# Optimization experiments

Hardware: AMD Instinct MI355X
Metric: run time of the kernel (lower is better)

## Reference

```python
import jax, jax.numpy as jnp
import numpy as np

N_STATE = 1280
N_HEAD = 20
D_HEAD = N_STATE // N_HEAD  # 64
N_MLP = 4 * N_STATE         # 5120
EPS = 1e-5


def _layer_norm(x, gamma, beta):
    mu = jnp.mean(x, axis=-1, keepdims=True)
    var = jnp.mean(jnp.square(x - mu), axis=-1, keepdims=True)
    return (x - mu) * jax.lax.rsqrt(var + EPS) * gamma + beta


def setup_inputs() -> dict:
    key = jax.random.key(0)
    ks = jax.random.split(key, 16)
    s = lambda fan_in: 1.0 / np.sqrt(fan_in)
    d = {
        "x": jax.random.normal(ks[0], (1, 1500, N_STATE), jnp.float32),
        # attention projections (stored [in, out]; torch Linear does x @ W.T + b)
        "Wq": jax.random.normal(ks[1], (N_STATE, N_STATE), jnp.float32) * s(N_STATE),
        "bq": jax.random.normal(ks[2], (N_STATE,), jnp.float32) * 0.02,
        "Wk": jax.random.normal(ks[3], (N_STATE, N_STATE), jnp.float32) * s(N_STATE),  # no bias
        "Wv": jax.random.normal(ks[4], (N_STATE, N_STATE), jnp.float32) * s(N_STATE),
        "bv": jax.random.normal(ks[5], (N_STATE,), jnp.float32) * 0.02,
        "Wo": jax.random.normal(ks[6], (N_STATE, N_STATE), jnp.float32) * s(N_STATE),
        "bo": jax.random.normal(ks[7], (N_STATE,), jnp.float32) * 0.02,
        # layer norms
        "ln1_g": jnp.ones((N_STATE,), jnp.float32),
        "ln1_b": jnp.zeros((N_STATE,), jnp.float32),
        "ln2_g": jnp.ones((N_STATE,), jnp.float32),
        "ln2_b": jnp.zeros((N_STATE,), jnp.float32),
        # MLP
        "W1": jax.random.normal(ks[8], (N_STATE, N_MLP), jnp.float32) * s(N_STATE),
        "b1": jax.random.normal(ks[9], (N_MLP,), jnp.float32) * 0.02,
        "W2": jax.random.normal(ks[10], (N_MLP, N_STATE), jnp.float32) * s(N_MLP),
        "b2": jax.random.normal(ks[11], (N_STATE,), jnp.float32) * 0.02,
    }
    return d


def reference(x, Wq, bq, Wk, Wv, bv, Wo, bo, ln1_g, ln1_b, ln2_g, ln2_b, W1, b1, W2, b2):
    B, S, C = x.shape
    scale = D_HEAD ** -0.5

    # --- multi-head self-attention ---
    h = _layer_norm(x, ln1_g, ln1_b)
    q = (h @ Wq + bq).reshape(B, S, N_HEAD, D_HEAD)
    k = (h @ Wk).reshape(B, S, N_HEAD, D_HEAD)
    v = (h @ Wv + bv).reshape(B, S, N_HEAD, D_HEAD)
    # scores: [B, H, Q, K]; softmax over keys (dim=1 'k' in the torch einsum)
    scores = jnp.einsum('bqhd,bkhd->bhqk', q, k) * scale
    w = jax.nn.softmax(scores, axis=-1)
    attn = jnp.einsum('bhqk,bkhd->bqhd', w, v).reshape(B, S, C)
    attn = attn @ Wo + bo
    x = x + attn

    # --- MLP (exact GELU, matching torch nn.GELU default) ---
    h2 = _layer_norm(x, ln2_g, ln2_b)
    h2 = jax.nn.gelu(h2 @ W1 + b1, approximate=False)
    x = x + (h2 @ W2 + b2)
    return x
```

## Files before the change

kernel.cpp:

```cpp
#include <hip/hip_runtime.h>
#include <hip/hip_bf16.h>
#include <math.h>

typedef __bf16 bf16x8 __attribute__((ext_vector_type(8)));
typedef float f32x4 __attribute__((ext_vector_type(4)));

#define SEQ 1500
#define CDIM 1280
#define NHEAD 20
#define DHEAD 64
#define NMLP 5120
#define QKVN 3840
#define VTLD 1504
#define APAD 68

#define GLOAD_LDS16(gp, lp)                                                    \
  __builtin_amdgcn_global_load_lds(                                            \
      (const __attribute__((address_space(1))) unsigned int*)(gp),             \
      (__attribute__((address_space(3))) unsigned int*)(lp), 16, 0, 0)

__global__ void detect_kernel(const unsigned int* __restrict__ xw,
                              int* __restrict__ flag) {
  __shared__ int cnt[256];
  const unsigned int w = xw[threadIdx.x];
  const unsigned int e = (w >> 7) & 0xFF;
  cnt[threadIdx.x] = (e >= 100 && e <= 150) ? 1 : 0;
  __syncthreads();
  for (int s = 128; s > 0; s >>= 1) {
    if (threadIdx.x < (unsigned)s) cnt[threadIdx.x] += cnt[threadIdx.x + s];
    __syncthreads();
  }
  if (threadIdx.x == 0) flag[0] = (cnt[0] >= 160) ? 1 : 0;
}

__global__ __launch_bounds__(256) void pack_params_kernel(
    const void* bq, const void* bv, const void* bo, const void* g1,
    const void* be1, const void* g2, const void* be2, const void* b1,
    const void* b2, __bf16* __restrict__ pb, const int* __restrict__ flag) {
  const int isbf = flag[0];
  const int i = blockIdx.x * 256 + threadIdx.x;
  if (i >= 16640) return;
  auto ld = [&](const void* p, int j) -> float {
    return isbf ? (float)((const __bf16*)p)[j] : ((const float*)p)[j];
  };
  float v;
  if (i < 3840) {
    if (i < 1280) v = ld(bq, i);
    else if (i < 2560) v = 0.f;
    else v = ld(bv, i - 2560);
  } else if (i < 5120) v = ld(bo, i - 3840);
  else if (i < 6400) v = ld(g1, i - 5120);
  else if (i < 7680) v = ld(be1, i - 6400);
  else if (i < 8960) v = ld(g2, i - 7680);
  else if (i < 10240) v = ld(be2, i - 8960);
  else if (i < 15360) v = ld(b1, i - 10240);
  else v = ld(b2, i - 15360);
  pb[i] = (__bf16)v;
}

__device__ __forceinline__ void transpose_body(const void* in, __bf16* out,
                                               int K, int N, int isbf) {
  __shared__ __bf16 t[32][33];
  const int tx = threadIdx.x, ty = threadIdx.y;
  const int n0 = blockIdx.x * 32, k0 = blockIdx.y * 32;
  if (isbf) {
    const __bf16* s = (const __bf16*)in;
#pragma unroll
    for (int i = ty; i < 32; i += 8)
      t[i][tx] = s[(size_t)(k0 + i) * N + n0 + tx];
  } else {
    const float* s = (const float*)in;
#pragma unroll
    for (int i = ty; i < 32; i += 8)
      t[i][tx] = (__bf16)s[(size_t)(k0 + i) * N + n0 + tx];
  }
  __syncthreads();
#pragma unroll
  for (int i = ty; i < 32; i += 8)
    out[(size_t)(n0 + i) * K + k0 + tx] = t[tx][i];
}

__global__ __launch_bounds__(256) void transpose_kernel(const void* __restrict__ in,
                                                        __bf16* __restrict__ out,
                                                        int K, int N,
                                                        const int* __restrict__ flag) {
  transpose_body(in, out, K, N, flag[0]);
}

__global__ __launch_bounds__(256) void transpose3_kernel(const void* __restrict__ Wq,
                                                         const void* __restrict__ Wk,
                                                         const void* __restrict__ Wv,
                                                         __bf16* __restrict__ out,
                                                         const int* __restrict__ flag) {
  const void* in = blockIdx.z == 0 ? Wq : (blockIdx.z == 1 ? Wk : Wv);
  transpose_body(in, out + (size_t)blockIdx.z * CDIM * CDIM, CDIM, CDIM, flag[0]);
}

__global__ __launch_bounds__(256) void transpose_act_kernel(const __bf16* __restrict__ in,
                                                            __bf16* __restrict__ out,
                                                            int istride) {
  __shared__ __bf16 t[32][33];
  const int tx = threadIdx.x, ty = threadIdx.y;
  const int n0 = blockIdx.x * 32, k0 = blockIdx.y * 32;
#pragma unroll
  for (int i = ty; i < 32; i += 8) {
    const int k = k0 + i;
    t[i][tx] = (k < SEQ) ? in[(size_t)k * istride + n0 + tx] : (__bf16)0.f;
  }
  __syncthreads();
#pragma unroll
  for (int i = ty; i < 32; i += 8) {
    const int kk = k0 + tx;
    if (kk < VTLD) out[(size_t)(n0 + i) * VTLD + kk] = t[tx][i];
  }
}

__global__ __launch_bounds__(256) void ln_kernel(const void* __restrict__ X,
                                                 const __bf16* __restrict__ gamma,
                                                 const __bf16* __restrict__ beta,
                                                 __bf16* __restrict__ Y,
                                                 int xflag, const int* __restrict__ flag) {
  const int isf32 = xflag ? (flag[0] == 0) : 0;
  const int row = blockIdx.x;
  float v[5];
  float s = 0.f, s2 = 0.f;
#pragma unroll
  for (int i = 0; i < 5; ++i) {
    const int c = threadIdx.x + 256 * i;
    const size_t idx = (size_t)row * CDIM + c;
    v[i] = isf32 ? ((const float*)X)[idx] : (float)((const __bf16*)X)[idx];
    s += v[i];
    s2 += v[i] * v[i];
  }
  const int lane = threadIdx.x & 63, wv = threadIdx.x >> 6;
#pragma unroll
  for (int off = 32; off > 0; off >>= 1) {
    s += __shfl_down(s, off);
    s2 += __shfl_down(s2, off);
  }
  __shared__ float red[8];
  if (lane == 0) { red[wv] = s; red[4 + wv] = s2; }
  __syncthreads();
  s = red[0] + red[1] + red[2] + red[3];
  s2 = red[4] + red[5] + red[6] + red[7];
  const float mu = s * (1.f / CDIM);
  const float var = s2 * (1.f / CDIM) - mu * mu;
  const float rstd = rsqrtf(fmaxf(var, 0.f) + 1e-5f);
#pragma unroll
  for (int i = 0; i < 5; ++i) {
    const int c = threadIdx.x + 256 * i;
    Y[(size_t)row * CDIM + c] =
        (__bf16)((v[i] - mu) * rstd * (float)gamma[c] + (float)beta[c]);
  }
}

__global__ __launch_bounds__(256) void gemm64_kernel(
    const __bf16* __restrict__ A, const __bf16* __restrict__ Bt,
    const __bf16* __restrict__ bias, void* __restrict__ Cv,
    int M, int N, int K, int KS, int gelu, int nsplit) {
  __shared__ __bf16 As[2][64 * 32];
  __shared__ __bf16 Bs[2][128 * 32];
  const int bm = blockIdx.x, bn = blockIdx.y, sz = blockIdx.z;
  const int tid = threadIdx.x;
  const int lane = tid & 63, wave = tid >> 6;
  const int l16 = lane & 15, kq = (lane >> 4) << 3;
  const int lrow = lane >> 2, lcol = (lane & 3) << 3;
  const int wn = wave * 32;

  f32x4 acc[4][2];
  const f32x4 zero = {0.f, 0.f, 0.f, 0.f};
#pragma unroll
  for (int i = 0; i < 4; ++i)
#pragma unroll
    for (int j = 0; j < 2; ++j) acc[i][j] = zero;

  const int kbeg = sz * KS;
  int kend = kbeg + KS;
  if (kend > K) kend = K;

  int ga = bm * 64 + wave * 16 + lrow;
  if (ga > M - 1) ga = M - 1;
  const __bf16* Ap = A + (size_t)ga * K + lcol;

  for (int k0 = kbeg; k0 < kend; k0 += 64) {
#pragma unroll
    for (int c = 0; c < 2; ++c)
      GLOAD_LDS16(Ap + k0 + c * 32, &As[c][wave * 512]);
#pragma unroll
    for (int c = 0; c < 2; ++c)
#pragma unroll
      for (int t = 0; t < 2; ++t) {
        const int seg = t * 4 + wave;
        const int gb = bn * 128 + seg * 16 + lrow;
        GLOAD_LDS16(Bt + (size_t)gb * K + k0 + c * 32 + lcol, &Bs[c][seg * 512]);
      }
    __syncthreads();
    bf16x8 af[4][2], bfr[2][2];
#pragma unroll
    for (int i = 0; i < 4; ++i)
#pragma unroll
      for (int c = 0; c < 2; ++c)
        af[i][c] = *(const bf16x8*)(&As[c][(i * 16 + l16) * 32 + kq]);
#pragma unroll
    for (int j = 0; j < 2; ++j)
#pragma unroll
      for (int c = 0; c < 2; ++c)
        bfr[j][c] = *(const bf16x8*)(&Bs[c][(wn + j * 16 + l16) * 32 + kq]);
#pragma unroll
    for (int i = 0; i < 4; ++i)
#pragma unroll
      for (int j = 0; j < 2; ++j)
#pragma unroll
        for (int c = 0; c < 2; ++c)
          acc[i][j] = __builtin_amdgcn_mfma_f32_16x16x32_bf16(af[i][c], bfr[j][c],
                                                              acc[i][j], 0, 0, 0);
    __syncthreads();
  }

  const int rq4 = (lane >> 4) * 4;
  if (nsplit > 1) {
    float* P = (float*)Cv + (size_t)sz * M * N;
#pragma unroll
    for (int i = 0; i < 4; ++i)
#pragma unroll
      for (int r = 0; r < 4; ++r) {
        const int grow = bm * 64 + i * 16 + rq4 + r;
        if (grow >= M) continue;
#pragma unroll
        for (int j = 0; j < 2; ++j) {
          const int gcol = bn * 128 + wn + j * 16 + l16;
          P[(size_t)grow * N + gcol] = acc[i][j][r];
        }
      }
  } else {
    __bf16* Cb = (__bf16*)Cv;
#pragma unroll
    for (int i = 0; i < 4; ++i)
#pragma unroll
      for (int r = 0; r < 4; ++r) {
        const int grow = bm * 64 + i * 16 + rq4 + r;
        if (grow >= M) continue;
#pragma unroll
        for (int j = 0; j < 2; ++j) {
          const int gcol = bn * 128 + wn + j * 16 + l16;
          float vv = acc[i][j][r];
          if (bias) vv += (float)bias[gcol];
          if (gelu) vv = 0.5f * vv * (1.f + erff(vv * 0.70710678118654752f));
          Cb[(size_t)grow * N + gcol] = (__bf16)vv;
        }
      }
  }
}

__global__ __launch_bounds__(256) void reduce_kernel(
    const float* __restrict__ P, const __bf16* __restrict__ bias,
    const void* __restrict__ resid, void* __restrict__ out,
    int MN, int N, int S, int residflagged, int outflagged,
    const int* __restrict__ flag) {
  const int i = blockIdx.x * 256 + threadIdx.x;
  if (i >= MN) return;
  float v = 0.f;
  for (int s = 0; s < S; ++s) v += P[(size_t)s * MN + i];
  v += (float)bias[i % N];
  if (resid) {
    const int rf32 = residflagged ? (flag[0] == 0) : 0;
    v += rf32 ? ((const float*)resid)[i] : (float)((const __bf16*)resid)[i];
  }
  const int outbf = outflagged ? flag[0] : 1;
  if (outbf) ((__bf16*)out)[i] = (__bf16)v;
  else       ((float*)out)[i] = v;
}

__global__ __launch_bounds__(256) void attn_mfma_kernel(
    const __bf16* __restrict__ Q,
    const __bf16* __restrict__ Kk,
    const __bf16* __restrict__ Vt,
    float* __restrict__ Opart,
    float* __restrict__ ml,
    int rs) {
  const int h = blockIdx.y;
  const int q0 = blockIdx.x * 64;
  const int z = blockIdx.z;
  const int tid = threadIdx.x;
  const int wave = tid >> 6, lane = tid & 63;
  const int l16 = lane & 15, quad = lane >> 4;

  __shared__ __bf16 Ks[64 * APAD];
  __shared__ __bf16 Vs[64 * APAD];
  __shared__ __bf16 Ps[4][16 * APAD];

  bf16x8 qf[2];
  {
    int q = q0 + wave * 16 + l16;
    if (q > SEQ - 1) q = SEQ - 1;
    const __bf16* qp = Q + (size_t)q * rs + h * DHEAD + quad * 8;
    qf[0] = *(const bf16x8*)(qp);
    qf[1] = *(const bf16x8*)(qp + 32);
  }

  f32x4 oacc[4];
  const f32x4 zero = {0.f, 0.f, 0.f, 0.f};
#pragma unroll
  for (int jt = 0; jt < 4; ++jt) oacc[jt] = zero;
  float mrow[4], lrow[4];
#pragma unroll
  for (int r = 0; r < 4; ++r) { mrow[r] = -30000.f; lrow[r] = 0.f; }

  const int srow = tid >> 2;
  const int scol = (tid & 3) << 4;

  const __bf16* Kbase = Kk + h * DHEAD;
  const __bf16* Vbase = Vt + (size_t)(h * DHEAD + srow) * VTLD;

  for (int kt = z * 12; kt < z * 12 + 12; ++kt) {
    const int key0 = kt * 64;
    __syncthreads();
    {
      int gk = key0 + srow;
      if (gk > SEQ - 1) gk = SEQ - 1;
      const __bf16* kp = Kbase + (size_t)gk * rs + scol;
      *(bf16x8*)(&Ks[srow * APAD + scol]) = *(const bf16x8*)(kp);
      *(bf16x8*)(&Ks[srow * APAD + scol + 8]) = *(const bf16x8*)(kp + 8);
      const __bf16* vp = Vbase + key0 + scol;
      *(bf16x8*)(&Vs[srow * APAD + scol]) = *(const bf16x8*)(vp);
      *(bf16x8*)(&Vs[srow * APAD + scol + 8]) = *(const bf16x8*)(vp + 8);
    }
    __syncthreads();

    f32x4 s[4];
#pragma unroll
    for (int jt = 0; jt < 4; ++jt) s[jt] = zero;
#pragma unroll
    for (int jt = 0; jt < 4; ++jt)
#pragma unroll
      for (int ks = 0; ks < 2; ++ks) {
        const bf16x8 kf = *(const bf16x8*)(&Ks[(jt * 16 + l16) * APAD + ks * 32 + quad * 8]);
        s[jt] = __builtin_amdgcn_mfma_f32_16x16x32_bf16(qf[ks], kf, s[jt], 0, 0, 0);
      }

#pragma unroll
    for (int jt = 0; jt < 4; ++jt) {
      const int key = key0 + jt * 16 + l16;
#pragma unroll
      for (int r = 0; r < 4; ++r) {
        float sv = s[jt][r] * 0.125f;
        if (key >= SEQ) sv = -30000.f;
        s[jt][r] = sv;
      }
    }

#pragma unroll
    for (int r = 0; r < 4; ++r) {
      float tmax = fmaxf(fmaxf(s[0][r], s[1][r]), fmaxf(s[2][r], s[3][r]));
#pragma unroll
      for (int off = 8; off > 0; off >>= 1) tmax = fmaxf(tmax, __shfl_xor(tmax, off));
      const float mnew = fmaxf(mrow[r], tmax);
      const float alpha = __expf(mrow[r] - mnew);
      mrow[r] = mnew;
      lrow[r] *= alpha;
#pragma unroll
      for (int jt = 0; jt < 4; ++jt) oacc[jt][r] *= alpha;
#pragma unroll
      for (int jt = 0; jt < 4; ++jt) {
        const float p = __expf(s[jt][r] - mnew);
        lrow[r] += p;
        Ps[wave][(quad * 4 + r) * APAD + jt * 16 + l16] = (__bf16)p;
      }
    }

    bf16x8 pf[2];
    pf[0] = *(const bf16x8*)(&Ps[wave][l16 * APAD + quad * 8]);
    pf[1] = *(const bf16x8*)(&Ps[wave][l16 * APAD + 32 + quad * 8]);
#pragma unroll
    for (int jt = 0; jt < 4; ++jt)
#pragma unroll
      for (int ks = 0; ks < 2; ++ks) {
        const bf16x8 vf = *(const bf16x8*)(&Vs[(jt * 16 + l16) * APAD + ks * 32 + quad * 8]);
        oacc[jt] = __builtin_amdgcn_mfma_f32_16x16x32_bf16(pf[ks], vf, oacc[jt], 0, 0, 0);
      }
  }

  float* Oz = Opart + (size_t)z * SEQ * CDIM;
#pragma unroll
  for (int r = 0; r < 4; ++r) {
    float lt = lrow[r];
#pragma unroll
    for (int off = 8; off > 0; off >>= 1) lt += __shfl_xor(lt, off);
    const int q = q0 + wave * 16 + quad * 4 + r;
    if (q < SEQ) {
#pragma unroll
      for (int jt = 0; jt < 4; ++jt)
        Oz[(size_t)q * CDIM + h * DHEAD + jt * 16 + l16] = oacc[jt][r];
      if (l16 == 0) {
        const size_t mi = ((size_t)(z * NHEAD + h) * SEQ + q) * 2;
        ml[mi] = mrow[r];
        ml[mi + 1] = lt;
      }
    }
  }
}

__global__ __launch_bounds__(256) void attn_combine_kernel(
    const float* __restrict__ Op, const float* __restrict__ ml,
    __bf16* __restrict__ O) {
  const int i = blockIdx.x * 256 + threadIdx.x;
  if (i >= SEQ * CDIM) return;
  const int q = i / CDIM;
  const int h = (i % CDIM) >> 6;
  const size_t m1i = ((size_t)h * SEQ + q) * 2;
  const size_t m2i = ((size_t)(NHEAD + h) * SEQ + q) * 2;
  const float m1 = ml[m1i], l1 = ml[m1i + 1];
  const float m2 = ml[m2i], l2 = ml[m2i + 1];
  const float M = fmaxf(m1, m2);
  const float e1 = __expf(m1 - M), e2 = __expf(m2 - M);
  const float v = (e1 * Op[i] + e2 * Op[(size_t)SEQ * CDIM + i]) /
                  (e1 * l1 + e2 * l2);
  O[i] = (__bf16)v;
}

extern "C" void kernel_launch(void* const* d_in, const int* in_sizes, int n_in,
                              void* d_out, int out_size, void* d_ws, size_t ws_size,
                              hipStream_t stream) {
  const void* x   = d_in[0];
  const void* Wq  = d_in[1];
  const void* bq  = d_in[2];
  const void* Wk  = d_in[3];
  const void* Wv  = d_in[4];
  const void* bv  = d_in[5];
  const void* Wo  = d_in[6];
  const void* bo  = d_in[7];
  const void* g1  = d_in[8];
  const void* be1 = d_in[9];
  const void* g2  = d_in[10];
  const void* be2 = d_in[11];
  const void* W1  = d_in[12];
  const void* bm1 = d_in[13];
  const void* W2  = d_in[14];
  const void* bm2 = d_in[15];

  char* ws = (char*)d_ws;
  size_t off = 0;
  auto alloc = [&](size_t elems) {
    __bf16* p = (__bf16*)(ws + off);
    off += elems * sizeof(__bf16);
    return p;
  };
  __bf16* Wqkvt = alloc((size_t)QKVN * CDIM);
  __bf16* Wot   = alloc((size_t)CDIM * CDIM);
  __bf16* W1t   = alloc((size_t)CDIM * NMLP);
  __bf16* W2t   = alloc((size_t)CDIM * NMLP);
  __bf16* qkvb  = alloc((size_t)SEQ * QKVN);
  __bf16* hb    = alloc((size_t)SEQ * CDIM);
  __bf16* mb    = alloc((size_t)SEQ * NMLP);
  __bf16* pb    = alloc(20480);
  off = (off + 15) & ~(size_t)15;
  float* pscr = (float*)(ws + off);
  off += (size_t)2 * SEQ * CDIM * sizeof(float);
  float* mlb = (float*)(ws + off);
  off += (size_t)2 * NHEAD * SEQ * 2 * sizeof(float);
  int* flag = (int*)(ws + off);

  __bf16* vtb  = mb;
  __bf16* x1b  = qkvb;
  __bf16* h2b  = qkvb + (size_t)SEQ * CDIM;

  __bf16* qkvbias = pb + 0;
  __bf16* bo_b  = pb + 3840;
  __bf16* g1_b  = pb + 5120;
  __bf16* be1_b = pb + 6400;
  __bf16* g2_b  = pb + 7680;
  __bf16* be2_b = pb + 8960;
  __bf16* b1_b  = pb + 10240;
  __bf16* b2_b  = pb + 15360;

  detect_kernel<<<1, 256, 0, stream>>>((const unsigned int*)x, flag);
  pack_params_kernel<<<65, 256, 0, stream>>>(bq, bv, bo, g1, be1, g2, be2,
                                             bm1, bm2, pb, flag);

  const dim3 tb(32, 8);
  transpose3_kernel<<<dim3(40, 40, 3), tb, 0, stream>>>(Wq, Wk, Wv, Wqkvt, flag);
  transpose_kernel<<<dim3(40, 40), tb, 0, stream>>>(Wo, Wot, CDIM, CDIM, flag);
  transpose_kernel<<<dim3(160, 40), tb, 0, stream>>>(W1, W1t, CDIM, NMLP, flag);
  transpose_kernel<<<dim3(40, 160), tb, 0, stream>>>(W2, W2t, NMLP, CDIM, flag);

  ln_kernel<<<SEQ, 256, 0, stream>>>(x, g1_b, be1_b, hb, 1, flag);
  gemm64_kernel<<<dim3(24, 30, 1), 256, 0, stream>>>(
      hb, Wqkvt, qkvbias, qkvb, SEQ, QKVN, CDIM, CDIM, 0, 1);
  transpose_act_kernel<<<dim3(40, 47), tb, 0, stream>>>(qkvb + 2560, vtb, QKVN);
  attn_mfma_kernel<<<dim3(24, NHEAD, 2), 256, 0, stream>>>(
      qkvb, qkvb + 1280, vtb, pscr, mlb, QKVN);
  attn_combine_kernel<<<7500, 256, 0, stream>>>(pscr, mlb, hb);
  gemm64_kernel<<<dim3(24, 10, 2), 256, 0, stream>>>(
      hb, Wot, nullptr, pscr, SEQ, CDIM, CDIM, 640, 0, 2);
  reduce_kernel<<<7500, 256, 0, stream>>>(pscr, bo_b, x, x1b,
                                          SEQ * CDIM, CDIM, 2, 1, 0, flag);
  ln_kernel<<<SEQ, 256, 0, stream>>>(x1b, g2_b, be2_b, h2b, 0, flag);
  gemm64_kernel<<<dim3(24, 40, 1), 256, 0, stream>>>(
      h2b, W1t, b1_b, mb, SEQ, NMLP, CDIM, CDIM, 1, 1);
  gemm64_kernel<<<dim3(24, 10, 2), 256, 0, stream>>>(
      mb, W2t, nullptr, pscr, SEQ, CDIM, NMLP, 2560, 0, 2);
  reduce_kernel<<<7500, 256, 0, stream>>>(pscr, b2_b, x1b, d_out,
                                          SEQ * CDIM, CDIM, 2, 0, 1, flag);
}
```

Before: 377.2 us.

## Add 128x128 double-buffered GEMM for QKV/MLP1 and prefetch in split-K GEMM

Adds a new 128x128-tile GEMM kernel with a 2x2 wave layout, used for the QKV projection and the first MLP GEMM, so each wave computes a 64x64 sub-tile and reuses its LDS fragments more. Both that kernel and the existing split-K 64x128 GEMM now use 32-wide K steps with a double-buffered LDS prefetch: the next tile is loaded while the current one is computed, and there is one barrier per iteration. This targets global-load latency stalls and barrier overhead. The trade-off is fewer blocks for the large GEMMs (360/480 blocks), which lowers occupancy and wave-level parallelism, plus higher register pressure from 16 accumulators.

```diff
diff --git a/kernel.cpp b/kernel.cpp
--- a/kernel.cpp
+++ b/kernel.cpp
@@ -154,10 +154,86 @@
   }
 }
 
+__global__ __launch_bounds__(256) void gemm128_kernel(
+    const __bf16* __restrict__ A, const __bf16* __restrict__ Bt,
+    const __bf16* __restrict__ bias, __bf16* __restrict__ C,
+    int M, int N, int K, int gelu) {
+  __shared__ __bf16 As[2][128 * 32];
+  __shared__ __bf16 Bs[2][128 * 32];
+  const int bm = blockIdx.x, bn = blockIdx.y;
+  const int tid = threadIdx.x;
+  const int lane = tid & 63, wave = tid >> 6;
+  const int wm = (wave >> 1) * 64, wn = (wave & 1) * 64;
+  const int l16 = lane & 15, kq = (lane >> 4) << 3;
+  const int lrow = lane >> 2, lcol = (lane & 3) << 3;
+
+  f32x4 acc[4][4];
+  const f32x4 zero = {0.f, 0.f, 0.f, 0.f};
+#pragma unroll
+  for (int i = 0; i < 4; ++i)
+#pragma unroll
+    for (int j = 0; j < 4; ++j) acc[i][j] = zero;
+
+  int ga0 = bm * 128 + wave * 16 + lrow;
+  if (ga0 > M - 1) ga0 = M - 1;
+  int ga1 = bm * 128 + (wave + 4) * 16 + lrow;
+  if (ga1 > M - 1) ga1 = M - 1;
+  const int gb0 = bn * 128 + wave * 16 + lrow;
+  const int gb1 = bn * 128 + (wave + 4) * 16 + lrow;
+  const __bf16* Ap0 = A + (size_t)ga0 * K + lcol;
+  const __bf16* Ap1 = A + (size_t)ga1 * K + lcol;
+  const __bf16* Bp0 = Bt + (size_t)gb0 * K + lcol;
+  const __bf16* Bp1 = Bt + (size_t)gb1 * K + lcol;
+
+  auto stage = [&](int b, int k0) {
+    GLOAD_LDS16(Ap0 + k0, &As[b][wave * 512]);
+    GLOAD_LDS16(Ap1 + k0, &As[b][(wave + 4) * 512]);
+    GLOAD_LDS16(Bp0 + k0, &Bs[b][wave * 512]);
+    GLOAD_LDS16(Bp1 + k0, &Bs[b][(wave + 4) * 512]);
+  };
+
+  stage(0, 0);
+  int buf = 0;
+  for (int k0 = 0; k0 < K; k0 += 32) {
+    __syncthreads();
+    if (k0 + 32 < K) stage(buf ^ 1, k0 + 32);
+    bf16x8 af[4], bfr[4];
+#pragma unroll
+    for (int i = 0; i < 4; ++i)
+      af[i] = *(const bf16x8*)(&As[buf][(wm + i * 16 + l16) * 32 + kq]);
+#pragma unroll
+    for (int j = 0; j < 4; ++j)
+      bfr[j] = *(const bf16x8*)(&Bs[buf][(wn + j * 16 + l16) * 32 + kq]);
+#pragma unroll
+    for (int i = 0; i < 4; ++i)
+#pragma unroll
+      for (int j = 0; j < 4; ++j)
+        acc[i][j] = __builtin_amdgcn_mfma_f32_16x16x32_bf16(af[i], bfr[j],
+                                                            acc[i][j], 0, 0, 0);
+    buf ^= 1;
+  }
+
+  const int rq4 = (lane >> 4) * 4;
+#pragma unroll
+  for (int i = 0; i < 4; ++i)
+#pragma unroll
+    for (int r = 0; r < 4; ++r) {
+      const int grow = bm * 128 + wm + i * 16 + rq4 + r;
+      if (grow >= M) continue;
+#pragma unroll
+      for (int j = 0; j < 4; ++j) {
+        const int gcol = bn * 128 + wn + j * 16 + l16;
+        float vv = acc[i][j][r];
+        if (bias) vv += (float)bias[gcol];
+        if (gelu) vv = 0.5f * vv * (1.f + erff(vv * 0.70710678118654752f));
+        C[(size_t)grow * N + gcol] = (__bf16)vv;
+      }
+    }
+}
+
 __global__ __launch_bounds__(256) void gemm64_kernel(
     const __bf16* __restrict__ A, const __bf16* __restrict__ Bt,
-    const __bf16* __restrict__ bias, void* __restrict__ Cv,
-    int M, int N, int K, int KS, int gelu, int nsplit) {
+    float* __restrict__ P, int M, int N, int K, int KS) {
   __shared__ __bf16 As[2][64 * 32];
   __shared__ __bf16 Bs[2][128 * 32];
   const int bm = blockIdx.x, bn = blockIdx.y, sz = blockIdx.z;
@@ -180,76 +256,53 @@
 
   int ga = bm * 64 + wave * 16 + lrow;
   if (ga > M - 1) ga = M - 1;
+  const int gb0 = bn * 128 + wave * 16 + lrow;
+  const int gb1 = bn * 128 + (wave + 4) * 16 + lrow;
   const __bf16* Ap = A + (size_t)ga * K + lcol;
-
-  for (int k0 = kbeg; k0 < kend; k0 += 64) {
-#pragma unroll
-    for (int c = 0; c < 2; ++c)
-      GLOAD_LDS16(Ap + k0 + c * 32, &As[c][wave * 512]);
-#pragma unroll
-    for (int c = 0; c < 2; ++c)
-#pragma unroll
-      for (int t = 0; t < 2; ++t) {
-        const int seg = t * 4 + wave;
-        const int gb = bn * 128 + seg * 16 + lrow;
-        GLOAD_LDS16(Bt + (size_t)gb * K + k0 + c * 32 + lcol, &Bs[c][seg * 512]);
-      }
+  const __bf16* Bp0 = Bt + (size_t)gb0 * K + lcol;
+  const __bf16* Bp1 = Bt + (size_t)gb1 * K + lcol;
+
+  auto stage = [&](int b, int k0) {
+    GLOAD_LDS16(Ap + k0, &As[b][wave * 512]);
+    GLOAD_LDS16(Bp0 + k0, &Bs[b][wave * 512]);
+    GLOAD_LDS16(Bp1 + k0, &Bs[b][(wave + 4) * 512]);
+  };
+
+  stage(0, kbeg);
+  int buf = 0;
+  for (int k0 = kbeg; k0 < kend; k0 += 32) {
     __syncthreads();
-    bf16x8 af[4][2], bfr[2][2];
+    if (k0 + 32 < kend) stage(buf ^ 1, k0 + 32);
+    bf16x8 af[4], bfr[2];
 #pragma unroll
     for (int i = 0; i < 4; ++i)
-#pragma unroll
-      for (int c = 0; c < 2; ++c)
-        af[i][c] = *(const bf16x8*)(&As[c][(i * 16 + l16) * 32 + kq]);
+      af[i] = *(const bf16x8*)(&As[buf][(i * 16 + l16) * 32 + kq]);
 #pragma unroll
     for (int j = 0; j < 2; ++j)
-#pragma unroll
-      for (int c = 0; c < 2; ++c)
-        bfr[j][c] = *(const bf16x8*)(&Bs[c][(wn + j * 16 + l16) * 32 + kq]);
+      bfr[j] = *(const bf16x8*)(&Bs[buf][(wn + j * 16 + l16) * 32 + kq]);
 #pragma unroll
     for (int i = 0; i < 4; ++i)
 #pragma unroll
       for (int j = 0; j < 2; ++j)
-#pragma unroll
-        for (int c = 0; c < 2; ++c)
-          acc[i][j] = __builtin_amdgcn_mfma_f32_16x16x32_bf16(af[i][c], bfr[j][c],
-                                                              acc[i][j], 0, 0, 0);
-    __syncthreads();
-  }
-
+        acc[i][j] = __builtin_amdgcn_mfma_f32_16x16x32_bf16(af[i], bfr[j],
+                                                            acc[i][j], 0, 0, 0);
+    buf ^= 1;
+  }
+
+  float* Pz = P + (size_t)sz * M * N;
   const int rq4 = (lane >> 4) * 4;
-  if (nsplit > 1) {
-    float* P = (float*)Cv + (size_t)sz * M * N;
-#pragma unroll
-    for (int i = 0; i < 4; ++i)
-#pragma unroll
-      for (int r = 0; r < 4; ++r) {
-        const int grow = bm * 64 + i * 16 + rq4 + r;
-        if (grow >= M) continue;
-#pragma unroll
-        for (int j = 0; j < 2; ++j) {
-          const int gcol = bn * 128 + wn + j * 16 + l16;
-          P[(size_t)grow * N + gcol] = acc[i][j][r];
-        }
-      }
-  } else {
-    __bf16* Cb = (__bf16*)Cv;
-#pragma unroll
-    for (int i = 0; i < 4; ++i)
-#pragma unroll
-      for (int r = 0; r < 4; ++r) {
-        const int grow = bm * 64 + i * 16 + rq4 + r;
-        if (grow >= M) continue;
-#pragma unroll
-        for (int j = 0; j < 2; ++j) {
-          const int gcol = bn * 128 + wn + j * 16 + l16;
-          float vv = acc[i][j][r];
-          if (bias) vv += (float)bias[gcol];
-          if (gelu) vv = 0.5f * vv * (1.f + erff(vv * 0.70710678118654752f));
-          Cb[(size_t)grow * N + gcol] = (__bf16)vv;
-        }
-      }
-  }
+#pragma unroll
+  for (int i = 0; i < 4; ++i)
+#pragma unroll
+    for (int r = 0; r < 4; ++r) {
+      const int grow = bm * 64 + i * 16 + rq4 + r;
+      if (grow >= M) continue;
+#pragma unroll
+      for (int j = 0; j < 2; ++j) {
+        const int gcol = bn * 128 + wn + j * 16 + l16;
+        Pz[(size_t)grow * N + gcol] = acc[i][j][r];
+      }
+    }
 }
 
 __global__ __launch_bounds__(256) void reduce_kernel(
@@ -484,21 +537,21 @@
   transpose_kernel<<<dim3(40, 160), tb, 0, stream>>>(W2, W2t, NMLP, CDIM, flag);
 
   ln_kernel<<<SEQ, 256, 0, stream>>>(x, g1_b, be1_b, hb, 1, flag);
-  gemm64_kernel<<<dim3(24, 30, 1), 256, 0, stream>>>(
-      hb, Wqkvt, qkvbias, qkvb, SEQ, QKVN, CDIM, CDIM, 0, 1);
+  gemm128_kernel<<<dim3(12, 30), 256, 0, stream>>>(
+      hb, Wqkvt, qkvbias, qkvb, SEQ, QKVN, CDIM, 0);
   transpose_act_kernel<<<dim3(40, 47), tb, 0, stream>>>(qkvb + 2560, vtb, QKVN);
   attn_mfma_kernel<<<dim3(24, NHEAD, 2), 256, 0, stream>>>(
       qkvb, qkvb + 1280, vtb, pscr, mlb, QKVN);
   attn_combine_kernel<<<7500, 256, 0, stream>>>(pscr, mlb, hb);
   gemm64_kernel<<<dim3(24, 10, 2), 256, 0, stream>>>(
-      hb, Wot, nullptr, pscr, SEQ, CDIM, CDIM, 640, 0, 2);
+      hb, Wot, pscr, SEQ, CDIM, CDIM, 640);
   reduce_kernel<<<7500, 256, 0, stream>>>(pscr, bo_b, x, x1b,
                                           SEQ * CDIM, CDIM, 2, 1, 0, flag);
   ln_kernel<<<SEQ, 256, 0, stream>>>(x1b, g2_b, be2_b, h2b, 0, flag);
-  gemm64_kernel<<<dim3(24, 40, 1), 256, 0, stream>>>(
-      h2b, W1t, b1_b, mb, SEQ, NMLP, CDIM, CDIM, 1, 1);
+  gemm128_kernel<<<dim3(12, 40), 256, 0, stream>>>(
+      h2b, W1t, b1_b, mb, SEQ, NMLP, CDIM, 1);
   gemm64_kernel<<<dim3(24, 10, 2), 256, 0, stream>>>(
-      mb, W2t, nullptr, pscr, SEQ, CDIM, NMLP, 2560, 0, 2);
+      mb, W2t, pscr, SEQ, CDIM, NMLP, 2560);
   reduce_kernel<<<7500, 256, 0, stream>>>(pscr, b2_b, x1b, d_out,
                                           SEQ * CDIM, CDIM, 2, 0, 1, flag);
 }
```

After: 399.6 us. 1.06x slower.

## Use 128x128 GEMM tiles with LDS double buffering and XCD-aware block mapping

Applied to the files above, without the earlier changes.

Replaces the 64x128 GEMM kernel with a 128x128 tile in which each of four waves computes a 64x64 sub-tile. Global-to-LDS loads for the next K step are issued into a second buffer before computing the current one, which removes one barrier per iteration. A 1D grid is remapped so that consecutive block IDs, which land on different XCDs, take different N tiles while sharing the same M tile. The larger tile raises data reuse but halves block count (for example 384 blocks for QKV), doubles LDS use and adds accumulator registers, which may lower occupancy.

```diff
diff --git a/kernel.cpp b/kernel.cpp
--- a/kernel.cpp
+++ b/kernel.cpp
@@ -154,67 +154,87 @@
   }
 }
 
-__global__ __launch_bounds__(256) void gemm64_kernel(
+__global__ __launch_bounds__(256) void gemm128s_kernel(
     const __bf16* __restrict__ A, const __bf16* __restrict__ Bt,
     const __bf16* __restrict__ bias, void* __restrict__ Cv,
-    int M, int N, int K, int KS, int gelu, int nsplit) {
-  __shared__ __bf16 As[2][64 * 32];
-  __shared__ __bf16 Bs[2][128 * 32];
-  const int bm = blockIdx.x, bn = blockIdx.y, sz = blockIdx.z;
+    int M, int N, int K, int KS, int gelu, int nsplit,
+    int mtiles, int ntpad) {
+  __shared__ __bf16 As[2][2][128 * 32];
+  __shared__ __bf16 Bs[2][2][128 * 32];
+
+  int id = blockIdx.x;
+  const int per = mtiles * ntpad;
+  const int sz = id / per;
+  id %= per;
+  const int xcd = id & 7;
+  const int grp = id >> 3;
+  const int bm = grp % mtiles;
+  const int bn = (grp / mtiles) * 8 + xcd;
+  if (bn >= (N >> 7)) return;
+
   const int tid = threadIdx.x;
   const int lane = tid & 63, wave = tid >> 6;
+  const int wm = (wave >> 1) * 64, wn = (wave & 1) * 64;
   const int l16 = lane & 15, kq = (lane >> 4) << 3;
   const int lrow = lane >> 2, lcol = (lane & 3) << 3;
-  const int wn = wave * 32;
-
-  f32x4 acc[4][2];
+
+  f32x4 acc[4][4];
   const f32x4 zero = {0.f, 0.f, 0.f, 0.f};
 #pragma unroll
   for (int i = 0; i < 4; ++i)
 #pragma unroll
-    for (int j = 0; j < 2; ++j) acc[i][j] = zero;
+    for (int j = 0; j < 4; ++j) acc[i][j] = zero;
+
+  const __bf16* Ap[2];
+  const __bf16* Bp[2];
+#pragma unroll
+  for (int t = 0; t < 2; ++t) {
+    int ga = bm * 128 + t * 64 + wave * 16 + lrow;
+    if (ga > M - 1) ga = M - 1;
+    Ap[t] = A + (size_t)ga * K + lcol;
+    const int gb = bn * 128 + t * 64 + wave * 16 + lrow;
+    Bp[t] = Bt + (size_t)gb * K + lcol;
+  }
 
   const int kbeg = sz * KS;
   int kend = kbeg + KS;
   if (kend > K) kend = K;
 
-  int ga = bm * 64 + wave * 16 + lrow;
-  if (ga > M - 1) ga = M - 1;
-  const __bf16* Ap = A + (size_t)ga * K + lcol;
-
+  auto stage = [&](int b, int k0) {
+#pragma unroll
+    for (int t = 0; t < 2; ++t)
+#pragma unroll
+      for (int c = 0; c < 2; ++c) {
+        GLOAD_LDS16(Ap[t] + k0 + c * 32, &As[b][c][(t * 64 + wave * 16) * 32]);
+        GLOAD_LDS16(Bp[t] + k0 + c * 32, &Bs[b][c][(t * 64 + wave * 16) * 32]);
+      }
+  };
+
+  stage(0, kbeg);
+  int buf = 0;
   for (int k0 = kbeg; k0 < kend; k0 += 64) {
-#pragma unroll
-    for (int c = 0; c < 2; ++c)
-      GLOAD_LDS16(Ap + k0 + c * 32, &As[c][wave * 512]);
-#pragma unroll
-    for (int c = 0; c < 2; ++c)
-#pragma unroll
-      for (int t = 0; t < 2; ++t) {
-        const int seg = t * 4 + wave;
-        const int gb = bn * 128 + seg * 16 + lrow;
-        GLOAD_LDS16(Bt + (size_t)gb * K + k0 + c * 32 + lcol, &Bs[c][seg * 512]);
-      }
     __syncthreads();
-    bf16x8 af[4][2], bfr[2][2];
+    if (k0 + 64 < kend) stage(buf ^ 1, k0 + 64);
+    bf16x8 af[4][2], bfr[4][2];
 #pragma unroll
     for (int i = 0; i < 4; ++i)
 #pragma unroll
       for (int c = 0; c < 2; ++c)
-        af[i][c] = *(const bf16x8*)(&As[c][(i * 16 + l16) * 32 + kq]);
-#pragma unroll
-    for (int j = 0; j < 2; ++j)
+        af[i][c] = *(const bf16x8*)(&As[buf][c][(wm + i * 16 + l16) * 32 + kq]);
+#pragma unroll
+    for (int j = 0; j < 4; ++j)
 #pragma unroll
       for (int c = 0; c < 2; ++c)
-        bfr[j][c] = *(const bf16x8*)(&Bs[c][(wn + j * 16 + l16) * 32 + kq]);
+        bfr[j][c] = *(const bf16x8*)(&Bs[buf][c][(wn + j * 16 + l16) * 32 + kq]);
 #pragma unroll
     for (int i = 0; i < 4; ++i)
 #pragma unroll
-      for (int j = 0; j < 2; ++j)
+      for (int j = 0; j < 4; ++j)
 #pragma unroll
         for (int c = 0; c < 2; ++c)
           acc[i][j] = __builtin_amdgcn_mfma_f32_16x16x32_bf16(af[i][c], bfr[j][c],
                                                               acc[i][j], 0, 0, 0);
-    __syncthreads();
+    buf ^= 1;
   }
 
   const int rq4 = (lane >> 4) * 4;
@@ -224,10 +244,10 @@
     for (int i = 0; i < 4; ++i)
 #pragma unroll
       for (int r = 0; r < 4; ++r) {
-        const int grow = bm * 64 + i * 16 + rq4 + r;
+        const int grow = bm * 128 + wm + i * 16 + rq4 + r;
         if (grow >= M) continue;
 #pragma unroll
-        for (int j = 0; j < 2; ++j) {
+        for (int j = 0; j < 4; ++j) {
           const int gcol = bn * 128 + wn + j * 16 + l16;
           P[(size_t)grow * N + gcol] = acc[i][j][r];
         }
@@ -238,10 +258,10 @@
     for (int i = 0; i < 4; ++i)
 #pragma unroll
       for (int r = 0; r < 4; ++r) {
-        const int grow = bm * 64 + i * 16 + rq4 + r;
+        const int grow = bm * 128 + wm + i * 16 + rq4 + r;
         if (grow >= M) continue;
 #pragma unroll
-        for (int j = 0; j < 2; ++j) {
+        for (int j = 0; j < 4; ++j) {
           const int gcol = bn * 128 + wn + j * 16 + l16;
           float vv = acc[i][j][r];
           if (bias) vv += (float)bias[gcol];
@@ -484,21 +504,21 @@
   transpose_kernel<<<dim3(40, 160), tb, 0, stream>>>(W2, W2t, NMLP, CDIM, flag);
 
   ln_kernel<<<SEQ, 256, 0, stream>>>(x, g1_b, be1_b, hb, 1, flag);
-  gemm64_kernel<<<dim3(24, 30, 1), 256, 0, stream>>>(
-      hb, Wqkvt, qkvbias, qkvb, SEQ, QKVN, CDIM, CDIM, 0, 1);
+  gemm128s_kernel<<<12 * 32, 256, 0, stream>>>(
+      hb, Wqkvt, qkvbias, qkvb, SEQ, QKVN, CDIM, CDIM, 0, 1, 12, 32);
   transpose_act_kernel<<<dim3(40, 47), tb, 0, stream>>>(qkvb + 2560, vtb, QKVN);
   attn_mfma_kernel<<<dim3(24, NHEAD, 2), 256, 0, stream>>>(
       qkvb, qkvb + 1280, vtb, pscr, mlb, QKVN);
   attn_combine_kernel<<<7500, 256, 0, stream>>>(pscr, mlb, hb);
-  gemm64_kernel<<<dim3(24, 10, 2), 256, 0, stream>>>(
-      hb, Wot, nullptr, pscr, SEQ, CDIM, CDIM, 640, 0, 2);
+  gemm128s_kernel<<<12 * 16 * 2, 256, 0, stream>>>(
+      hb, Wot, nullptr, pscr, SEQ, CDIM, CDIM, 640, 0, 2, 12, 16);
   reduce_kernel<<<7500, 256, 0, stream>>>(pscr, bo_b, x, x1b,
                                           SEQ * CDIM, CDIM, 2, 1, 0, flag);
   ln_kernel<<<SEQ, 256, 0, stream>>>(x1b, g2_b, be2_b, h2b, 0, flag);
-  gemm64_kernel<<<dim3(24, 40, 1), 256, 0, stream>>>(
-      h2b, W1t, b1_b, mb, SEQ, NMLP, CDIM, CDIM, 1, 1);
-  gemm64_kernel<<<dim3(24, 10, 2), 256, 0, stream>>>(
-      mb, W2t, nullptr, pscr, SEQ, CDIM, NMLP, 2560, 0, 2);
+  gemm128s_kernel<<<12 * 40, 256, 0, stream>>>(
+      h2b, W1t, b1_b, mb, SEQ, NMLP, CDIM, CDIM, 1, 1, 12, 40);
+  gemm128s_kernel<<<12 * 16 * 2, 256, 0, stream>>>(
+      mb, W2t, nullptr, pscr, SEQ, CDIM, NMLP, 2560, 0, 2, 12, 16);
   reduce_kernel<<<7500, 256, 0, stream>>>(pscr, b2_b, x1b, d_out,
                                           SEQ * CDIM, CDIM, 2, 0, 1, flag);
 }
```

New measurement: 395.3 us. 4.8% more time.
